# Kernel optimization log

Hardware: AMD Instinct MI355X
Metric: run time of the kernel (lower is better)

Reference implementation:

```python
import jax, jax.numpy as jnp
import numpy as np
import math

D_MODEL = 256
N_LEVELS = 4
N_HEADS = 8
N_POINTS = 4
N_FRAME = 4
SHAPES = [(80, 80), (40, 40), (20, 20), (10, 10)]  # sum H*W = 8500
NB = 2
T1 = 4
T2 = 4
LEN_Q = 8500


def _grid_init_bias():
    # replicate torch _reset_parameters grid bias for sampling_offsets
    thetas = np.arange(N_HEADS, dtype=np.float32) * (2.0 * math.pi / N_HEADS)
    grid = np.stack([np.cos(thetas), np.sin(thetas)], -1)
    grid = grid / np.abs(grid).max(-1, keepdims=True)
    grid = np.tile(grid[:, None, None, :], (1, N_LEVELS, N_POINTS, 1))
    grid = grid * (np.arange(N_POINTS, dtype=np.float32) + 1.0)[None, None, :, None]
    return jnp.asarray(grid.reshape(-1), jnp.float32)


def setup_inputs() -> dict:
    key = jax.random.key(0)
    ks = jax.random.split(key, 8)
    Len_in = sum(h * w for h, w in SHAPES)
    query = jax.random.normal(ks[0], (NB, T1, LEN_Q, D_MODEL), jnp.float32)
    reference_points = jax.random.uniform(ks[1], (NB, T1, LEN_Q, N_LEVELS, 2), jnp.float32)
    input_flatten = jax.random.normal(ks[2], (NB, T2, Len_in, D_MODEL), jnp.float32)
    input_spatial_shapes = jnp.array(SHAPES, jnp.int32)
    starts = np.cumsum([0] + [h * w for h, w in SHAPES])[:-1]
    input_level_start_index = jnp.asarray(starts, jnp.int32)
    s = 0.01
    W_off = jax.random.normal(ks[3], (D_MODEL, N_HEADS * N_LEVELS * N_POINTS * 2), jnp.float32) * s
    b_off = _grid_init_bias()
    W_att = jax.random.normal(ks[4], (D_MODEL, N_HEADS * N_LEVELS * N_POINTS), jnp.float32) * s
    b_att = jnp.zeros((N_HEADS * N_LEVELS * N_POINTS,), jnp.float32)
    xav = 1.0 / math.sqrt(D_MODEL)
    W_val = jax.random.normal(ks[5], (D_MODEL, D_MODEL), jnp.float32) * xav
    b_val = jnp.zeros((D_MODEL,), jnp.float32)
    W_out = jax.random.normal(ks[6], (D_MODEL, D_MODEL), jnp.float32) * xav
    b_out = jnp.zeros((D_MODEL,), jnp.float32)
    return dict(query=query, reference_points=reference_points, input_flatten=input_flatten,
                input_spatial_shapes=input_spatial_shapes, input_level_start_index=input_level_start_index,
                W_off=W_off, b_off=b_off, W_att=W_att, b_att=b_att,
                W_val=W_val, b_val=b_val, W_out=W_out, b_out=b_out)


def _bilinear(v_flat, H, W, gx, gy):
    # v_flat: (B, d, H*W); gx,gy: (B, S) in [-1,1]; zeros padding, align_corners=False
    x = (gx + 1.0) * (W * 0.5) - 0.5
    y = (gy + 1.0) * (H * 0.5) - 0.5
    x0 = jnp.floor(x); y0 = jnp.floor(y)
    x1 = x0 + 1.0; y1 = y0 + 1.0
    wx1 = x - x0; wx0 = 1.0 - wx1
    wy1 = y - y0; wy0 = 1.0 - wy1

    def gather(xi, yi):
        valid = ((xi >= 0) & (xi < W) & (yi >= 0) & (yi < H)).astype(v_flat.dtype)
        xc = jnp.clip(xi, 0, W - 1).astype(jnp.int32)
        yc = jnp.clip(yi, 0, H - 1).astype(jnp.int32)
        idx = yc * W + xc  # (B, S)
        g = jnp.take_along_axis(v_flat, idx[:, None, :], axis=2)  # (B, d, S)
        return g * valid[:, None, :]

    return (gather(x0, y0) * (wx0 * wy0)[:, None, :]
            + gather(x1, y0) * (wx1 * wy0)[:, None, :]
            + gather(x0, y1) * (wx0 * wy1)[:, None, :]
            + gather(x1, y1) * (wx1 * wy1)[:, None, :])


def _core(value_t, locs, att, shapes):
    # value_t: (n, Len_in, M, d); locs: (n, Lq, M, L, P, 2); att: (n, Lq, M, L, P)
    n, Len_in, M, d = value_t.shape
    Lq, P = locs.shape[1], locs.shape[4]
    start = 0
    out = 0.0
    for l, (H, W) in enumerate(shapes):
        hw = H * W
        v = value_t[:, start:start + hw]  # (n, hw, M, d)
        start += hw
        v = v.transpose(0, 2, 3, 1).reshape(n * M, d, hw)
        g = locs[:, :, :, l] * 2.0 - 1.0  # (n, Lq, M, P, 2)
        g = g.transpose(0, 2, 1, 3, 4).reshape(n * M, Lq * P, 2)
        samp = _bilinear(v, H, W, g[..., 0], g[..., 1])  # (n*M, d, Lq*P)
        a = att[:, :, :, l].transpose(0, 2, 1, 3).reshape(n * M, 1, Lq * P)
        out = out + (samp * a).reshape(n, M, d, Lq, P).sum(-1)
    return out.transpose(0, 3, 1, 2).reshape(n, Lq, M * d)  # (n, Lq, C)


def reference(query, reference_points, input_flatten, input_spatial_shapes, input_level_start_index,
              W_off, b_off, W_att, b_att, W_val, b_val, W_out, b_out):
    shapes = [(int(h), int(w)) for h, w in np.asarray(input_spatial_shapes)]
    n, t1n, Lq, C = query.shape
    M, L, P = N_HEADS, N_LEVELS, N_POINTS
    d = C // M
    value = input_flatten @ W_val + b_val  # (n, T2, Len_in, C)
    value = value.reshape(n, value.shape[1], -1, M, d)
    normalizer = jnp.array([[w, h] for h, w in shapes], jnp.float32)  # (L, 2) = (W_l, H_l)
    outs = []
    for t1 in range(t1n):
        t2s = [t for t in (t1 - 1, t1, t1 + 1) if 0 <= t < N_FRAME]
        K = len(t2s)
        q = query[:, t1]  # (n, Lq, C)
        # all frames share ONE attention_weights Linear -> identical logits per t2
        logits = (q @ W_att + b_att).reshape(n, Lq, M, L, P)
        stacked = jnp.broadcast_to(logits[..., None], (n, Lq, M, L, P, K))
        att = jax.nn.softmax(stacked.reshape(n, Lq, M, L * P * K), axis=-1)
        att = att.reshape(n, Lq, M, L, P, K)
        # all frames share ONE sampling_offsets Linear -> identical locations per t2
        off = (q @ W_off + b_off).reshape(n, Lq, M, L, P, 2)
        off = off / normalizer[None, None, None, :, None, :]
        locs = reference_points[:, t1][:, :, None, :, None, :] + off  # (n,Lq,M,L,P,2)
        out_t1 = 0.0
        for k, t2 in enumerate(t2s):
            out_t1 = out_t1 + _core(value[:, t2], locs, att[..., k], shapes)
        outs.append(out_t1)
    out = jnp.stack(outs, axis=1)  # (n, T1, Lq, C)
    return out @ W_out + b_out
```

## Files before the change

### kernel.cpp

```cpp
#include <hip/hip_runtime.h>

#define LQ 8500

typedef _Float16 half8 __attribute__((ext_vector_type(8)));
typedef float f32x4 __attribute__((ext_vector_type(4)));

__device__ __forceinline__ unsigned short f2h(float f) {
    return __builtin_bit_cast(unsigned short, (_Float16)f);
}
__device__ __forceinline__ float hlo(unsigned w) {
    return (float)__builtin_bit_cast(_Float16, (unsigned short)(w & 0xffffu));
}
__device__ __forceinline__ float hhi(unsigned w) {
    return (float)__builtin_bit_cast(_Float16, (unsigned short)(w >> 16));
}
__device__ __forceinline__ unsigned pk2(float a, float b) {
    return (unsigned)f2h(a) | ((unsigned)f2h(b) << 16);
}

__device__ __forceinline__ void gl_lds16(const unsigned short* gsrc, char* ldst) {
    __builtin_amdgcn_global_load_lds(
        (const __attribute__((address_space(1))) void*)gsrc,
        (__attribute__((address_space(3))) void*)ldst, 16, 0, 0);
}

__global__ __launch_bounds__(256) void prep_weights(const float* __restrict__ Woff,
                                                    const float* __restrict__ boff,
                                                    const float* __restrict__ Watt,
                                                    const float* __restrict__ batt,
                                                    const float* __restrict__ Wval,
                                                    const float* __restrict__ Wout,
                                                    unsigned short* __restrict__ Wct,
                                                    unsigned short* __restrict__ Wvt,
                                                    unsigned short* __restrict__ Wot,
                                                    float* __restrict__ bcat) {
    int idx = blockIdx.x * 256 + threadIdx.x;
    if (idx < 98304) {
        int j = idx >> 8, k = idx & 255;
        float v = (j < 256) ? Woff[k * 256 + j] : Watt[k * 128 + (j - 256)];
        Wct[idx] = f2h(v);
    } else if (idx < 98304 + 65536) {
        int t = idx - 98304;
        int n = t >> 8, k = t & 255;
        Wvt[t] = f2h(Wval[k * 256 + n]);
    } else if (idx < 98304 + 131072) {
        int t = idx - 98304 - 65536;
        int n = t >> 8, k = t & 255;
        Wot[t] = f2h(Wout[k * 256 + n]);
    } else if (idx < 98304 + 131072 + 384) {
        int j = idx - 98304 - 131072;
        bcat[j] = (j < 256) ? boff[j] : batt[j - 256];
    }
}

__device__ __forceinline__ void inv_swz(int d, int& brow, int& bseg) {
    int b8 = (d >> 8) & 1;
    int rm = (((d >> 6) & 1) ^ b8) | (((d >> 7) & 1) << 1) | (b8 << 2);
    int b = d ^ (rm << 4);
    brow = b >> 6;
    bseg = (b >> 4) & 3;
}

__global__ __launch_bounds__(256) void gemm_yp(const float* __restrict__ inp,
                                               const float* __restrict__ query,
                                               const unsigned short* __restrict__ Wvt,
                                               const unsigned short* __restrict__ Wct,
                                               const float* __restrict__ bcat,
                                               unsigned short* __restrict__ Yo,
                                               unsigned short* __restrict__ Po) {
    __shared__ char lds[32768];
    const int tid = threadIdx.x;
    const int r0 = blockIdx.x * 128;
    const int yb = blockIdx.y;
    const bool isY = yb < 2;
    const int c0 = isY ? yb * 128 : (yb - 2) * 128;
    const float* A = isY ? inp : query;
    const unsigned short* Bt = isY ? Wvt : Wct;
    const int wid = tid >> 6, lane = tid & 63;
    const int wr = (wid >> 1) * 64, wc = (wid & 1) * 64;
    const int M = 8 * LQ;

    int browc[2], bsegc[2];
#pragma unroll
    for (int cc = 0; cc < 2; ++cc)
        inv_swz((cc * 256 + tid) << 4, browc[cc], bsegc[cc]);

    f32x4 acc[4][4] = {};
    uint4 ra[2];

#define LOADA(k0)                                                                   \
    {                                                                               \
        _Pragma("unroll")                                                           \
        for (int cc = 0; cc < 2; ++cc) {                                            \
            int ch = cc * 256 + tid;                                               \
            int row = ch >> 2, seg = ch & 3;                                        \
            uint4 va = {0, 0, 0, 0};                                               \
            int ar = r0 + row;                                                      \
            if (ar < M) {                                                           \
                const float4* ap = reinterpret_cast<const float4*>(                 \
                    A + (size_t)ar * 256 + (k0) + seg * 8);                         \
                float4 a = ap[0], b = ap[1];                                        \
                va.x = pk2(a.x, a.y); va.y = pk2(a.z, a.w);                         \
                va.z = pk2(b.x, b.y); va.w = pk2(b.z, b.w);                         \
            }                                                                       \
            ra[cc] = va;                                                            \
        }                                                                           \
    }

#define STOREA(bf)                                                                  \
    {                                                                               \
        _Pragma("unroll")                                                           \
        for (int cc = 0; cc < 2; ++cc) {                                            \
            int ch = cc * 256 + tid;                                               \
            int row = ch >> 2, seg = ch & 3;                                        \
            int byte = (row << 6) + (seg << 4);                                     \
            int swzb = byte ^ ((row & 7) << 4);                                     \
            *reinterpret_cast<uint4*>(lds + (bf) * 16384 + swzb) = ra[cc];          \
        }                                                                           \
    }

#define LOADB(bf, k0)                                                               \
    {                                                                               \
        _Pragma("unroll")                                                           \
        for (int cc = 0; cc < 2; ++cc) {                                            \
            const unsigned short* gs =                                              \
                Bt + (size_t)(c0 + browc[cc]) * 256 + (k0) + bsegc[cc] * 8;         \
            gl_lds16(gs, lds + (bf) * 16384 + 8192 + cc * 4096 + wid * 1024);       \
        }                                                                           \
    }

    LOADA(0);
    LOADB(0, 0);
    STOREA(0);
    __syncthreads();

    for (int t = 0; t < 8; ++t) {
        if (t < 7) {
            LOADB((t + 1) & 1, (t + 1) * 32);
            LOADA((t + 1) * 32);
        }
        char* base = lds + (t & 1) * 16384;
        half8 af[4], bfr[4];
#pragma unroll
        for (int i = 0; i < 4; ++i) {
            int rowA = wr + i * 16 + (lane & 15);
            int byteA = (rowA << 6) + ((lane >> 4) << 4);
            af[i] = *reinterpret_cast<const half8*>(base + (byteA ^ ((rowA & 7) << 4)));
            int rowB = wc + i * 16 + (lane & 15);
            int byteB = (rowB << 6) + ((lane >> 4) << 4);
            bfr[i] = *reinterpret_cast<const half8*>(base + 8192 + (byteB ^ ((rowB & 7) << 4)));
        }
#pragma unroll
        for (int i = 0; i < 4; ++i)
#pragma unroll
            for (int j = 0; j < 4; ++j)
                acc[i][j] = __builtin_amdgcn_mfma_f32_16x16x32_f16(af[i], bfr[j], acc[i][j], 0, 0, 0);
        if (t < 7) STOREA((t + 1) & 1);
        __syncthreads();
    }

#pragma unroll
    for (int j = 0; j < 4; ++j) {
        int col = c0 + wc + j * 16 + (lane & 15);
        float bv = isY ? 0.f : bcat[col];
#pragma unroll
        for (int i = 0; i < 4; ++i) {
#pragma unroll
            for (int r = 0; r < 4; ++r) {
                int row = r0 + wr + i * 16 + (lane >> 4) * 4 + r;
                if (row >= M) continue;
                float v = acc[i][j][r] + bv;
                if (isY) Yo[(size_t)row * 256 + col] = f2h(v);
                else     Po[(size_t)row * 384 + col] = f2h(v);
            }
        }
    }
#undef LOADA
#undef STOREA
#undef LOADB
}

__global__ __launch_bounds__(256) void gemm_out(const unsigned short* __restrict__ O16,
                                                const unsigned short* __restrict__ Wot,
                                                const float* __restrict__ bout,
                                                float* __restrict__ out) {
    __shared__ char lds[32768];
    const int tid = threadIdx.x;
    const int r0 = blockIdx.x * 128, c0 = blockIdx.y * 128;
    const int wid = tid >> 6, lane = tid & 63;
    const int wr = (wid >> 1) * 64, wc = (wid & 1) * 64;
    const int M = 8 * LQ;

    int browc[2], bsegc[2];
#pragma unroll
    for (int cc = 0; cc < 2; ++cc)
        inv_swz((cc * 256 + tid) << 4, browc[cc], bsegc[cc]);

    f32x4 acc[4][4] = {};

#define STAGE(bf, k0)                                                               \
    {                                                                               \
        _Pragma("unroll")                                                           \
        for (int cc = 0; cc < 2; ++cc) {                                            \
            char* lbase = lds + (bf) * 16384 + cc * 4096 + wid * 1024;              \
            int ar = r0 + browc[cc];                                                \
            if (ar < M)                                                             \
                gl_lds16(O16 + (size_t)ar * 256 + (k0) + bsegc[cc] * 8, lbase);     \
            gl_lds16(Wot + (size_t)(c0 + browc[cc]) * 256 + (k0) + bsegc[cc] * 8,   \
                     lbase + 8192);                                                 \
        }                                                                           \
    }

    STAGE(0, 0);
    __syncthreads();

    for (int t = 0; t < 8; ++t) {
        if (t < 7) STAGE((t + 1) & 1, (t + 1) * 32);
        char* base = lds + (t & 1) * 16384;
        half8 af[4], bfr[4];
#pragma unroll
        for (int i = 0; i < 4; ++i) {
            int rowA = wr + i * 16 + (lane & 15);
            int byteA = (rowA << 6) + ((lane >> 4) << 4);
            af[i] = *reinterpret_cast<const half8*>(base + (byteA ^ ((rowA & 7) << 4)));
            int rowB = wc + i * 16 + (lane & 15);
            int byteB = (rowB << 6) + ((lane >> 4) << 4);
            bfr[i] = *reinterpret_cast<const half8*>(base + 8192 + (byteB ^ ((rowB & 7) << 4)));
        }
#pragma unroll
        for (int i = 0; i < 4; ++i)
#pragma unroll
            for (int j = 0; j < 4; ++j)
                acc[i][j] = __builtin_amdgcn_mfma_f32_16x16x32_f16(af[i], bfr[j], acc[i][j], 0, 0, 0);
        __syncthreads();
    }

#pragma unroll
    for (int j = 0; j < 4; ++j) {
        int col = c0 + wc + j * 16 + (lane & 15);
        float bv = bout[col];
#pragma unroll
        for (int i = 0; i < 4; ++i) {
#pragma unroll
            for (int r = 0; r < 4; ++r) {
                int row = r0 + wr + i * 16 + (lane >> 4) * 4 + r;
                if (row >= M) continue;
                out[(size_t)row * 256 + col] = acc[i][j][r] + bv;
            }
        }
    }
#undef STAGE
}

__global__ __launch_bounds__(256) void vsum_kernel(const unsigned short* __restrict__ Y,
                                                   const float* __restrict__ bval,
                                                   unsigned short* __restrict__ Vs) {
    int plane = blockIdx.y;
    int g = plane >> 3, m = plane & 7;
    int t1 = g & 3, n = g >> 2;
    int f = blockIdx.x * 256 + threadIdx.x;
    if (f >= LQ * 4) return;
    int pos = f >> 2, c8 = (f & 3) * 8;
    float Kc = (t1 == 0 || t1 == 3) ? 2.f : 3.f;
    const float* bp = bval + m * 32 + c8;
    float acc[8];
#pragma unroll
    for (int j = 0; j < 8; ++j) acc[j] = Kc * bp[j];
    int t2a = t1 == 0 ? 0 : t1 - 1;
    int t2b = t1 == 3 ? 3 : t1 + 1;
    for (int t2 = t2a; t2 <= t2b; ++t2) {
        uint4 v = *reinterpret_cast<const uint4*>(
            Y + ((size_t)(n * 4 + t2) * LQ + pos) * 256 + m * 32 + c8);
        acc[0] += hlo(v.x); acc[1] += hhi(v.x);
        acc[2] += hlo(v.y); acc[3] += hhi(v.y);
        acc[4] += hlo(v.z); acc[5] += hhi(v.z);
        acc[6] += hlo(v.w); acc[7] += hhi(v.w);
    }
    uint4 o;
    o.x = pk2(acc[0], acc[1]); o.y = pk2(acc[2], acc[3]);
    o.z = pk2(acc[4], acc[5]); o.w = pk2(acc[6], acc[7]);
    *reinterpret_cast<uint4*>(Vs + ((size_t)plane * LQ + pos) * 32 + c8) = o;
}

__global__ __launch_bounds__(256) void sample_kernel(const unsigned short* __restrict__ P,
                                                     const float* __restrict__ refp,
                                                     const unsigned short* __restrict__ Vs,
                                                     unsigned short* __restrict__ O16) {
    int tid = threadIdx.x, bid = blockIdx.x;
    int g = bid & 7;
    int q0 = (bid >> 3) * 16;
    int ql = tid >> 4, m = (tid >> 1) & 7, h = tid & 1;
    int q = q0 + ql;
    if (q >= LQ) return;

    const size_t qrow = (size_t)g * LQ + q;

    unsigned ow[16];
    {
        const uint4* po = reinterpret_cast<const uint4*>(P + qrow * 384 + m * 32);
        uint4 a = po[0], b = po[1], c = po[2], d = po[3];
        ow[0] = a.x; ow[1] = a.y; ow[2] = a.z; ow[3] = a.w;
        ow[4] = b.x; ow[5] = b.y; ow[6] = b.z; ow[7] = b.w;
        ow[8] = c.x; ow[9] = c.y; ow[10] = c.z; ow[11] = c.w;
        ow[12] = d.x; ow[13] = d.y; ow[14] = d.z; ow[15] = d.w;
    }
    float wgt[16];
    {
        const uint4* pa = reinterpret_cast<const uint4*>(P + qrow * 384 + 256 + m * 16);
        uint4 a = pa[0], b = pa[1];
        unsigned aw[8] = {a.x, a.y, a.z, a.w, b.x, b.y, b.z, b.w};
#pragma unroll
        for (int j = 0; j < 8; ++j) {
            wgt[j * 2 + 0] = hlo(aw[j]);
            wgt[j * 2 + 1] = hhi(aw[j]);
        }
        float mx = -1e30f;
#pragma unroll
        for (int j = 0; j < 16; ++j) mx = fmaxf(mx, wgt[j]);
        float s = 0.f;
#pragma unroll
        for (int j = 0; j < 16; ++j) { wgt[j] = __expf(wgt[j] - mx); s += wgt[j]; }
        int t1 = g & 3;
        float Kc = (t1 == 0 || t1 == 3) ? 2.f : 3.f;
        float inv = 1.f / (s * Kc);
#pragma unroll
        for (int j = 0; j < 16; ++j) wgt[j] *= inv;
    }

    float rx[4], ry[4];
    {
        const float4* rp = reinterpret_cast<const float4*>(refp + qrow * 8);
        float4 r0 = rp[0], r1 = rp[1];
        rx[0] = r0.x; ry[0] = r0.y; rx[1] = r0.z; ry[1] = r0.w;
        rx[2] = r1.x; ry[2] = r1.y; rx[3] = r1.z; ry[3] = r1.w;
    }

    float acc[16];
#pragma unroll
    for (int d = 0; d < 16; ++d) acc[d] = 0.f;

    const unsigned short* vplane = Vs + (size_t)(g * 8 + m) * (LQ * 32) + h * 16;

#pragma unroll 4
    for (int p = 0; p < 16; ++p) {
        const int l = p >> 2;
        const int Wl = 80 >> l;
        const int start = (l == 0) ? 0 : (l == 1) ? 6400 : (l == 2) ? 8000 : 8400;
        const float Wlf = (float)Wl;

        float x = fmaf(rx[l], Wlf, hlo(ow[p])) - 0.5f;
        float y = fmaf(ry[l], Wlf, hhi(ow[p])) - 0.5f;
        float w = wgt[p];

        float xf = floorf(x), yf = floorf(y);
        int x0 = (int)xf, y0 = (int)yf;
        float wx1 = x - xf, wy1 = y - yf;

        int xb = min(max(x0, 0), Wl - 2);
        float wl = (x0 == xb) ? 1.f - wx1 : ((x0 + 1 == xb) ? wx1 : 0.f);
        float wr = (x0 == xb) ? wx1 : ((x0 - 1 == xb) ? 1.f - wx1 : 0.f);

        int yc0 = min(max(y0, 0), Wl - 1);
        float cw0 = (y0 >= 0 && y0 < Wl) ? (1.f - wy1) * w : 0.f;
        int y1i = y0 + 1;
        int yc1 = min(max(y1i, 0), Wl - 1);
        float cw1 = (y1i >= 0 && y1i < Wl) ? wy1 * w : 0.f;

        const uint4* p0 = reinterpret_cast<const uint4*>(
            vplane + (size_t)(start + yc0 * Wl + xb) * 32);
        const uint4* p1 = reinterpret_cast<const uint4*>(
            vplane + (size_t)(start + yc1 * Wl + xb) * 32);
        uint4 L0a = p0[0], L0b = p0[1], R0a = p0[4], R0b = p0[5];
        uint4 L1a = p1[0], L1b = p1[1], R1a = p1[4], R1b = p1[5];

        float c0l = cw0 * wl, c0r = cw0 * wr;
        float c1l = cw1 * wl, c1r = cw1 * wr;

        acc[0]  += c0l * hlo(L0a.x) + c0r * hlo(R0a.x) + c1l * hlo(L1a.x) + c1r * hlo(R1a.x);
        acc[1]  += c0l * hhi(L0a.x) + c0r * hhi(R0a.x) + c1l * hhi(L1a.x) + c1r * hhi(R1a.x);
        acc[2]  += c0l * hlo(L0a.y) + c0r * hlo(R0a.y) + c1l * hlo(L1a.y) + c1r * hlo(R1a.y);
        acc[3]  += c0l * hhi(L0a.y) + c0r * hhi(R0a.y) + c1l * hhi(L1a.y) + c1r * hhi(R1a.y);
        acc[4]  += c0l * hlo(L0a.z) + c0r * hlo(R0a.z) + c1l * hlo(L1a.z) + c1r * hlo(R1a.z);
        acc[5]  += c0l * hhi(L0a.z) + c0r * hhi(R0a.z) + c1l * hhi(L1a.z) + c1r * hhi(R1a.z);
        acc[6]  += c0l * hlo(L0a.w) + c0r * hlo(R0a.w) + c1l * hlo(L1a.w) + c1r * hlo(R1a.w);
        acc[7]  += c0l * hhi(L0a.w) + c0r * hhi(R0a.w) + c1l * hhi(L1a.w) + c1r * hhi(R1a.w);
        acc[8]  += c0l * hlo(L0b.x) + c0r * hlo(R0b.x) + c1l * hlo(L1b.x) + c1r * hlo(R1b.x);
        acc[9]  += c0l * hhi(L0b.x) + c0r * hhi(R0b.x) + c1l * hhi(L1b.x) + c1r * hhi(R1b.x);
        acc[10] += c0l * hlo(L0b.y) + c0r * hlo(R0b.y) + c1l * hlo(L1b.y) + c1r * hlo(R1b.y);
        acc[11] += c0l * hhi(L0b.y) + c0r * hhi(R0b.y) + c1l * hhi(L1b.y) + c1r * hhi(R1b.y);
        acc[12] += c0l * hlo(L0b.z) + c0r * hlo(R0b.z) + c1l * hlo(L1b.z) + c1r * hlo(R1b.z);
        acc[13] += c0l * hhi(L0b.z) + c0r * hhi(R0b.z) + c1l * hhi(L1b.z) + c1r * hhi(R1b.z);
        acc[14] += c0l * hlo(L0b.w) + c0r * hlo(R0b.w) + c1l * hlo(L1b.w) + c1r * hlo(R1b.w);
        acc[15] += c0l * hhi(L0b.w) + c0r * hhi(R0b.w) + c1l * hhi(L1b.w) + c1r * hhi(R1b.w);
    }

    unsigned short* op = O16 + qrow * 256 + m * 32 + h * 16;
    uint4 o0, o1;
    o0.x = pk2(acc[0], acc[1]);   o0.y = pk2(acc[2], acc[3]);
    o0.z = pk2(acc[4], acc[5]);   o0.w = pk2(acc[6], acc[7]);
    o1.x = pk2(acc[8], acc[9]);   o1.y = pk2(acc[10], acc[11]);
    o1.z = pk2(acc[12], acc[13]); o1.w = pk2(acc[14], acc[15]);
    reinterpret_cast<uint4*>(op)[0] = o0;
    reinterpret_cast<uint4*>(op)[1] = o1;
}

extern "C" void kernel_launch(void* const* d_in, const int* in_sizes, int n_in,
                              void* d_out, int out_size, void* d_ws, size_t ws_size,
                              hipStream_t stream) {
    const float* query = (const float*)d_in[0];
    const float* refp  = (const float*)d_in[1];
    const float* inp   = (const float*)d_in[2];
    const float* Woff = (const float*)d_in[5];
    const float* boff = (const float*)d_in[6];
    const float* Watt = (const float*)d_in[7];
    const float* batt = (const float*)d_in[8];
    const float* Wval = (const float*)d_in[9];
    const float* bval = (const float*)d_in[10];
    const float* Wout = (const float*)d_in[11];
    const float* bout = (const float*)d_in[12];
    float* out = (float*)d_out;

    char* base = (char*)d_ws;
    unsigned short* Y    = (unsigned short*)base;
    unsigned short* O16  = (unsigned short*)base;
    unsigned short* Vs   = (unsigned short*)(base + 34816000);
    unsigned short* P    = (unsigned short*)(base + 69632000);
    unsigned short* Wct  = (unsigned short*)(base + 121856000);
    unsigned short* Wvt  = (unsigned short*)(base + 122052608);
    unsigned short* Wot  = (unsigned short*)(base + 122183680);
    float* bcat          = (float*)(base + 122314752);

    const int RT = (8 * LQ + 127) / 128;

    prep_weights<<<dim3(898), 256, 0, stream>>>(Woff, boff, Watt, batt, Wval, Wout,
                                                Wct, Wvt, Wot, bcat);

    gemm_yp<<<dim3(RT, 5), 256, 0, stream>>>(inp, query, Wvt, Wct, bcat, Y, P);

    vsum_kernel<<<dim3((LQ * 4 + 255) / 256, 64), 256, 0, stream>>>(Y, bval, Vs);

    sample_kernel<<<dim3(((LQ + 15) / 16) * 8), 256, 0, stream>>>(P, refp, Vs, O16);

    gemm_out<<<dim3(RT, 2), 256, 0, stream>>>(O16, Wot, bout, out);
}
```

Baseline: 310.0 us.

## Widen input GEMM tiles to full N so fp32 A is read once per row block

Replaces the combined 128x128-tile projection GEMM with a templated 512-thread kernel that covers the full output width per block (256 columns for the value projection, 384 for offsets/attention). It is launched twice, once per projection. Each fp32 A row block is now loaded and converted to fp16 once instead of 2 or 3 times, which cuts global reads of the large input tensors. In exchange each block needs more LDS and more accumulator registers, and the grid has fewer blocks, which may lower occupancy.

```diff
diff --git a/kernel.cpp b/kernel.cpp
--- a/kernel.cpp
+++ b/kernel.cpp
@@ -22,6 +22,14 @@
     __builtin_amdgcn_global_load_lds(
         (const __attribute__((address_space(1))) void*)gsrc,
         (__attribute__((address_space(3))) void*)ldst, 16, 0, 0);
+}
+
+__device__ __forceinline__ void inv_swz(int d, int& brow, int& bseg) {
+    int b8 = (d >> 8) & 1;
+    int rm = (((d >> 6) & 1) ^ b8) | (((d >> 7) & 1) << 1) | (b8 << 2);
+    int b = d ^ (rm << 4);
+    brow = b >> 6;
+    bseg = (b >> 4) & 3;
 }
 
 __global__ __launch_bounds__(256) void prep_weights(const float* __restrict__ Woff,
@@ -53,79 +61,62 @@
     }
 }
 
-__device__ __forceinline__ void inv_swz(int d, int& brow, int& bseg) {
-    int b8 = (d >> 8) & 1;
-    int rm = (((d >> 6) & 1) ^ b8) | (((d >> 7) & 1) << 1) | (b8 << 2);
-    int b = d ^ (rm << 4);
-    brow = b >> 6;
-    bseg = (b >> 4) & 3;
-}
-
-__global__ __launch_bounds__(256) void gemm_yp(const float* __restrict__ inp,
-                                               const float* __restrict__ query,
-                                               const unsigned short* __restrict__ Wvt,
-                                               const unsigned short* __restrict__ Wct,
-                                               const float* __restrict__ bcat,
-                                               unsigned short* __restrict__ Yo,
-                                               unsigned short* __restrict__ Po) {
-    __shared__ char lds[32768];
+template <int NJ, int BIAS>
+__global__ __launch_bounds__(512) void gemm_wide(const float* __restrict__ A,
+                                                 const unsigned short* __restrict__ Bt,
+                                                 const float* __restrict__ bias,
+                                                 unsigned short* __restrict__ C,
+                                                 int M) {
+    const int BN = NJ * 64;
+    const int BUFSZ = 8192 + BN * 64;
+    const int NBCH = BN * 4;
+    const int NC = NBCH / 512;
+    __shared__ char lds[2 * (8192 + NJ * 64 * 64)];
+
     const int tid = threadIdx.x;
     const int r0 = blockIdx.x * 128;
-    const int yb = blockIdx.y;
-    const bool isY = yb < 2;
-    const int c0 = isY ? yb * 128 : (yb - 2) * 128;
-    const float* A = isY ? inp : query;
-    const unsigned short* Bt = isY ? Wvt : Wct;
     const int wid = tid >> 6, lane = tid & 63;
-    const int wr = (wid >> 1) * 64, wc = (wid & 1) * 64;
-    const int M = 8 * LQ;
-
-    int browc[2], bsegc[2];
-#pragma unroll
-    for (int cc = 0; cc < 2; ++cc)
-        inv_swz((cc * 256 + tid) << 4, browc[cc], bsegc[cc]);
-
-    f32x4 acc[4][4] = {};
-    uint4 ra[2];
+    const int wr = (wid >> 2) * 64;
+    const int wc = (wid & 3) * (NJ * 16);
+
+    int browc[3], bsegc[3];
+#pragma unroll
+    for (int cc = 0; cc < NC; ++cc)
+        inv_swz((cc * 512 + tid) << 4, browc[cc], bsegc[cc]);
+
+    f32x4 acc[4][NJ] = {};
+    uint4 ra;
 
 #define LOADA(k0)                                                                   \
     {                                                                               \
-        _Pragma("unroll")                                                           \
-        for (int cc = 0; cc < 2; ++cc) {                                            \
-            int ch = cc * 256 + tid;                                               \
-            int row = ch >> 2, seg = ch & 3;                                        \
-            uint4 va = {0, 0, 0, 0};                                               \
-            int ar = r0 + row;                                                      \
-            if (ar < M) {                                                           \
-                const float4* ap = reinterpret_cast<const float4*>(                 \
-                    A + (size_t)ar * 256 + (k0) + seg * 8);                         \
-                float4 a = ap[0], b = ap[1];                                        \
-                va.x = pk2(a.x, a.y); va.y = pk2(a.z, a.w);                         \
-                va.z = pk2(b.x, b.y); va.w = pk2(b.z, b.w);                         \
-            }                                                                       \
-            ra[cc] = va;                                                            \
+        int row = tid >> 2, seg = tid & 3;                                          \
+        uint4 va = {0, 0, 0, 0};                                                    \
+        int ar = r0 + row;                                                          \
+        if (ar < M) {                                                               \
+            const float4* ap = reinterpret_cast<const float4*>(                     \
+                A + (size_t)ar * 256 + (k0) + seg * 8);                             \
+            float4 a = ap[0], b = ap[1];                                            \
+            va.x = pk2(a.x, a.y); va.y = pk2(a.z, a.w);                             \
+            va.z = pk2(b.x, b.y); va.w = pk2(b.z, b.w);                             \
         }                                                                           \
+        ra = va;                                                                    \
     }
 
 #define STOREA(bf)                                                                  \
     {                                                                               \
-        _Pragma("unroll")                                                           \
-        for (int cc = 0; cc < 2; ++cc) {                                            \
-            int ch = cc * 256 + tid;                                               \
-            int row = ch >> 2, seg = ch & 3;                                        \
-            int byte = (row << 6) + (seg << 4);                                     \
-            int swzb = byte ^ ((row & 7) << 4);                                     \
-            *reinterpret_cast<uint4*>(lds + (bf) * 16384 + swzb) = ra[cc];          \
-        }                                                                           \
+        int row = tid >> 2, seg = tid & 3;                                          \
+        int byte = (row << 6) + (seg << 4);                                         \
+        int swzb = byte ^ ((row & 7) << 4);                                         \
+        *reinterpret_cast<uint4*>(lds + (bf) * BUFSZ + swzb) = ra;                  \
     }
 
 #define LOADB(bf, k0)                                                               \
     {                                                                               \
         _Pragma("unroll")                                                           \
-        for (int cc = 0; cc < 2; ++cc) {                                            \
+        for (int cc = 0; cc < NC; ++cc) {                                           \
             const unsigned short* gs =                                              \
-                Bt + (size_t)(c0 + browc[cc]) * 256 + (k0) + bsegc[cc] * 8;         \
-            gl_lds16(gs, lds + (bf) * 16384 + 8192 + cc * 4096 + wid * 1024);       \
+                Bt + (size_t)browc[cc] * 256 + (k0) + bsegc[cc] * 8;                \
+            gl_lds16(gs, lds + (bf) * BUFSZ + 8192 + cc * 8192 + wid * 1024);       \
         }                                                                           \
     }
 
@@ -139,39 +130,40 @@
             LOADB((t + 1) & 1, (t + 1) * 32);
             LOADA((t + 1) * 32);
         }
-        char* base = lds + (t & 1) * 16384;
-        half8 af[4], bfr[4];
+        char* base = lds + (t & 1) * BUFSZ;
+        half8 af[4], bfr[NJ];
 #pragma unroll
         for (int i = 0; i < 4; ++i) {
             int rowA = wr + i * 16 + (lane & 15);
             int byteA = (rowA << 6) + ((lane >> 4) << 4);
             af[i] = *reinterpret_cast<const half8*>(base + (byteA ^ ((rowA & 7) << 4)));
-            int rowB = wc + i * 16 + (lane & 15);
+        }
+#pragma unroll
+        for (int j = 0; j < NJ; ++j) {
+            int rowB = wc + j * 16 + (lane & 15);
             int byteB = (rowB << 6) + ((lane >> 4) << 4);
-            bfr[i] = *reinterpret_cast<const half8*>(base + 8192 + (byteB ^ ((rowB & 7) << 4)));
+            bfr[j] = *reinterpret_cast<const half8*>(base + 8192 + (byteB ^ ((rowB & 7) << 4)));
         }
 #pragma unroll
         for (int i = 0; i < 4; ++i)
 #pragma unroll
-            for (int j = 0; j < 4; ++j)
+            for (int j = 0; j < NJ; ++j)
                 acc[i][j] = __builtin_amdgcn_mfma_f32_16x16x32_f16(af[i], bfr[j], acc[i][j], 0, 0, 0);
         if (t < 7) STOREA((t + 1) & 1);
         __syncthreads();
     }
 
 #pragma unroll
-    for (int j = 0; j < 4; ++j) {
-        int col = c0 + wc + j * 16 + (lane & 15);
-        float bv = isY ? 0.f : bcat[col];
+    for (int j = 0; j < NJ; ++j) {
+        int col = wc + j * 16 + (lane & 15);
+        float bv = BIAS ? bias[col] : 0.f;
 #pragma unroll
         for (int i = 0; i < 4; ++i) {
 #pragma unroll
             for (int r = 0; r < 4; ++r) {
                 int row = r0 + wr + i * 16 + (lane >> 4) * 4 + r;
                 if (row >= M) continue;
-                float v = acc[i][j][r] + bv;
-                if (isY) Yo[(size_t)row * 256 + col] = f2h(v);
-                else     Po[(size_t)row * 384 + col] = f2h(v);
+                C[(size_t)row * BN + col] = f2h(acc[i][j][r] + bv);
             }
         }
     }
@@ -435,7 +427,9 @@
     prep_weights<<<dim3(898), 256, 0, stream>>>(Woff, boff, Watt, batt, Wval, Wout,
                                                 Wct, Wvt, Wot, bcat);
 
-    gemm_yp<<<dim3(RT, 5), 256, 0, stream>>>(inp, query, Wvt, Wct, bcat, Y, P);
+    gemm_wide<4, 0><<<dim3(RT), 512, 0, stream>>>(inp, Wvt, bcat, Y, 8 * LQ);
+
+    gemm_wide<6, 1><<<dim3(RT), 512, 0, stream>>>(query, Wct, bcat, P, 8 * LQ);
 
     vsum_kernel<<<dim3((LQ * 4 + 255) / 256, 64), 256, 0, stream>>>(Y, bval, Vs);
 
```

Result: slower. 319.0 us (+2.9%).
